# Kernel tuning notes

Hardware: AMD Instinct MI355X
Metric: run time of the kernel (lower is better)

Reference implementation:

```python
import jax, jax.numpy as jnp
import numpy as np

BATCH, SEQ, CH, ORDER = 4, 8192, 512, 64


def setup_inputs() -> dict:
    key = jax.random.key(0)
    k1, k2, k3 = jax.random.split(key, 3)
    x = jax.random.normal(k1, (BATCH, SEQ, CH), dtype=jnp.float32)
    # RTF parameters: small init so the denominator polynomial 1 + sum a_i z^-i
    # stays well-conditioned (stable transfer function), as in the FSSM init.
    A = 0.01 * jax.random.normal(k2, (CH, ORDER), dtype=jnp.float32)
    B = 0.01 * jax.random.normal(k3, (CH, ORDER), dtype=jnp.float32)
    h0 = jnp.zeros((1,), dtype=jnp.float32)
    return {"x": x, "A": A, "B": B, "h0": h0}


def _rtf_kernel(A, B, L):
    # Evaluate H(z) = b(z)/a(z) at the L roots of unity, then irfft -> impulse response.
    C = A.shape[0]
    a = jnp.concatenate([jnp.ones((C, 1), A.dtype), A], axis=-1)  # (C, N+1), leading coeff 1
    a_f = jnp.fft.rfft(a, n=L, axis=-1)                           # (C, L//2+1)
    b_f = jnp.fft.rfft(B, n=L, axis=-1)
    return jnp.fft.irfft(b_f / a_f, n=L, axis=-1)                 # (C, L)


def reference(x, A, B, h0):
    Bt, L, C = x.shape
    K = _rtf_kernel(A, B, L)                                      # (C, L)
    n_fft = 2 * L                                                 # causal (linear) convolution
    x_f = jnp.fft.rfft(x, n=n_fft, axis=1)                        # (B, n_fft//2+1, C)
    k_f = jnp.fft.rfft(K, n=n_fft, axis=-1).T[None]               # (1, n_fft//2+1, C)
    h1 = jnp.fft.irfft(x_f * k_f, n=n_fft, axis=1)[:, :L]         # (B, L, C)
    y1 = h1 + h0 * x
    return jax.nn.gelu(y1)
```

## Files before the change

kernel.cpp:

```cpp
#include <hip/hip_runtime.h>
#include <stdint.h>

#define NBATCH 4
#define LSEQ   8192
#define CH     512
#define ORDER  64
#define KTAP   256

typedef _Float16 half8 __attribute__((ext_vector_type(8)));
typedef _Float16 f16x2 __attribute__((ext_vector_type(2)));
typedef float    f32x4 __attribute__((ext_vector_type(4)));

#define NW    9
#define AFRAG_HALFS  ((size_t)CH * NW * 64 * 8)
#define WS_NEED      (AFRAG_HALFS * 2)

#define XSW   1320
#define XROWB 2640
#define LOW   260
#define LOWB  1040
#define SMEMB (16 * XROWB)

__device__ __forceinline__ uint32_t packh2(_Float16 lo, _Float16 hi) {
    f16x2 v; v.x = lo; v.y = hi;
    return __builtin_bit_cast(uint32_t, v);
}

__global__ __launch_bounds__(256) void rtf_afrag(const float* __restrict__ A,
                                                 const float* __restrict__ B,
                                                 const float* __restrict__ h0,
                                                 _Float16* __restrict__ afr) {
    __shared__ float Ksh[4][KTAP];
    const int wv = threadIdx.x >> 6, lane = threadIdx.x & 63;
    const int c  = blockIdx.x * 4 + wv;
    const float a  = A[c * ORDER + lane];
    const float bc = B[c * ORDER + lane];
    const float h0v = h0[0];
    float s = 0.0f;
    for (int t = 0; t < KTAP; ++t) {
        const float s1 = __shfl(s, 0);
        const float bt = (t < ORDER) ? __shfl(bc, t) : 0.0f;
        const float y  = bt + s1;
        float su = __shfl_down(s, 1);
        if (lane == ORDER - 1) su = 0.0f;
        s = su - a * y;
        if (lane == 0) Ksh[wv][t] = (t == 0) ? (y + h0v) : y;
    }
    __syncthreads();
    const int i = lane & 15, g = lane >> 4;
    for (int w = 0; w < NW; ++w) {
        half8 hv;
#pragma unroll
        for (int e = 0; e < 8; ++e) {
            const int t = 32 * w + 15 + i - 8 * g - e;
            hv[e] = (_Float16)((t >= 0 && t < KTAP) ? Ksh[wv][t] : 0.0f);
        }
        *reinterpret_cast<half8*>(afr + ((size_t)(c * NW + w) * 64 + lane) * 8) = hv;
    }
}

__global__ __launch_bounds__(256) void fir_mfma(const float* __restrict__ x,
                                                const _Float16* __restrict__ afr,
                                                float* __restrict__ out) {
    __shared__ __align__(16) char smem[SMEMB];
    const int gid     = blockIdx.x;
    const int logical = (gid & 7) * 128 + (gid >> 3);
    const int chgrp   = logical >> 5;
    const int rem     = logical & 31;
    const int bb      = rem >> 3;
    const int tg      = rem & 7;
    const int n0      = tg * 1024;

    {
        const int cg = threadIdx.x & 3;
        const int pr = threadIdx.x >> 2;
        const float* xsrc = x + (size_t)bb * LSEQ * CH + chgrp * 16 + cg * 4;
#pragma unroll
        for (int it = 0; it < 11; ++it) {
            const int p = pr + 64 * it;
            if (p < 656) {
                const int r0 = n0 - 271 + 2 * p;
                float4 v0 = {0.f, 0.f, 0.f, 0.f}, v1 = v0;
                if (r0 >= 0 && r0 < LSEQ)
                    v0 = *reinterpret_cast<const float4*>(xsrc + (size_t)r0 * CH);
                if (r0 + 1 >= 0 && r0 + 1 < LSEQ)
                    v1 = *reinterpret_cast<const float4*>(xsrc + (size_t)(r0 + 1) * CH);
                char* base = smem + (size_t)(cg * 4) * XROWB + 4 * p;
                *reinterpret_cast<uint32_t*>(base + 0 * XROWB) =
                    packh2((_Float16)v0.x, (_Float16)v1.x);
                *reinterpret_cast<uint32_t*>(base + 1 * XROWB) =
                    packh2((_Float16)v0.y, (_Float16)v1.y);
                *reinterpret_cast<uint32_t*>(base + 2 * XROWB) =
                    packh2((_Float16)v0.z, (_Float16)v1.z);
                *reinterpret_cast<uint32_t*>(base + 3 * XROWB) =
                    packh2((_Float16)v0.w, (_Float16)v1.w);
            }
        }
    }
    __syncthreads();

    const int wid = threadIdx.x >> 6, lane = threadIdx.x & 63;
    const int j = lane & 15, g = lane >> 4;
    const int c0 = chgrp * 16 + wid * 4;
    const _Float16* af = afr + (size_t)lane * 8;

    f32x4 acc[4][4];
#pragma unroll
    for (int ti = 0; ti < 4; ++ti)
#pragma unroll
        for (int q = 0; q < 4; ++q) acc[ti][q] = (f32x4){0.f, 0.f, 0.f, 0.f};

#pragma unroll
    for (int w = 0; w < NW; ++w) {
        half8 a[4];
#pragma unroll
        for (int q = 0; q < 4; ++q)
            a[q] = *reinterpret_cast<const half8*>(af + (size_t)((c0 + q) * NW + w) * 512);
        const int base = 16 * j + 8 * g - 32 * w + 256;
#pragma unroll
        for (int ti = 0; ti < 4; ++ti) {
#pragma unroll
            for (int q = 0; q < 4; ++q) {
                const half8 bv = *reinterpret_cast<const half8*>(
                    smem + (size_t)(wid * 4 + q) * XROWB + 2 * (base + 256 * ti));
                acc[ti][q] = __builtin_amdgcn_mfma_f32_16x16x32_f16(a[q], bv, acc[ti][q], 0, 0, 0);
            }
        }
    }

    const int cq = threadIdx.x & 3;
    const int nq = threadIdx.x >> 2;
#pragma unroll
    for (int ti = 0; ti < 4; ++ti) {
        __syncthreads();
#pragma unroll
        for (int q = 0; q < 4; ++q) {
            f32x4 o;
#pragma unroll
            for (int r = 0; r < 4; ++r) {
                const float y  = acc[ti][q][r];
                const float m2 = y * y;
                const float wv = fmaf(m2, 0.14270963f, 1.5957691f);
                const float e  = __expf(y * wv);
                const float rc = __builtin_amdgcn_rcpf(e + 1.0f);
                o[r] = y - y * rc;
            }
            *reinterpret_cast<f32x4*>(smem + (size_t)(wid * 4 + q) * LOWB
                                      + 4 * (16 * j + 4 * g)) = o;
        }
        __syncthreads();
        float* ob = out + ((size_t)bb * LSEQ + n0 + ti * 256) * CH + chgrp * 16 + cq * 4;
#pragma unroll
        for (int it = 0; it < 4; ++it) {
            const int n = nq + 64 * it;
            float4 o;
            o.x = *reinterpret_cast<float*>(smem + (size_t)(cq * 4 + 0) * LOWB + 4 * n);
            o.y = *reinterpret_cast<float*>(smem + (size_t)(cq * 4 + 1) * LOWB + 4 * n);
            o.z = *reinterpret_cast<float*>(smem + (size_t)(cq * 4 + 2) * LOWB + 4 * n);
            o.w = *reinterpret_cast<float*>(smem + (size_t)(cq * 4 + 3) * LOWB + 4 * n);
            *reinterpret_cast<float4*>(ob + (size_t)n * CH) = o;
        }
    }
}

#define RINGF 32
#define CPBF  256
__global__ __launch_bounds__(ORDER) void rtf_impulse_fb(const float* __restrict__ A,
                                                        const float* __restrict__ B,
                                                        const float* __restrict__ h0,
                                                        float* __restrict__ kt4) {
    const int c = blockIdx.x, lane = threadIdx.x;
    const float a = A[c * ORDER + lane], bc = B[c * ORDER + lane], h0v = h0[0];
    float s = 0.0f;
    for (int t = 0; t < KTAP; ++t) {
        const float s1 = __shfl(s, 0);
        const float bt = (t < ORDER) ? __shfl(bc, t) : 0.0f;
        const float y  = bt + s1;
        float su = __shfl_down(s, 1);
        if (lane == ORDER - 1) su = 0.0f;
        s = su - a * y;
        if (lane == 0) kt4[((size_t)(t >> 2) * CH + c) * 4 + (t & 3)] = (t == 0) ? (y + h0v) : y;
    }
}
__global__ __launch_bounds__(CPBF) void fir_gelu_fb(const float* __restrict__ x,
                                                    const float* __restrict__ kt4,
                                                    float* __restrict__ out) {
    const int h = blockIdx.x;
    const int logical = ((h & 7) << 8) | (h >> 3);
    const int tile = logical & 255, sl = logical >> 8;
    const int cb = sl & 1, b = sl >> 1;
    const int c = cb * CPBF + threadIdx.x;
    const int n0 = tile * RINGF;
    const float* xb = x + (size_t)b * LSEQ * CH + c;
    const float4* kt4v = (const float4*)kt4;
    float acc[RINGF]; float ring[RINGF]; float px[2][8]; float kbuf[2][8];
#pragma unroll
    for (int r = 0; r < RINGF; ++r) acc[r] = 0.0f;
#pragma unroll
    for (int i = 0; i < RINGF; ++i) ring[i] = xb[(size_t)(n0 + i) * CH];
    {
        const float4 ka = kt4v[(size_t)0 * CH + c];
        const float4 kb = kt4v[(size_t)1 * CH + c];
        kbuf[0][0] = ka.x; kbuf[0][1] = ka.y; kbuf[0][2] = ka.z; kbuf[0][3] = ka.w;
        kbuf[0][4] = kb.x; kbuf[0][5] = kb.y; kbuf[0][6] = kb.z; kbuf[0][7] = kb.w;
#pragma unroll
        for (int g2 = 0; g2 < 8; ++g2) {
            const int m = n0 - 1 - g2;
            px[0][g2] = (m >= 0) ? xb[(size_t)m * CH] : 0.0f;
        }
    }
    for (int tb = 0; tb < KTAP; tb += RINGF) {
#pragma unroll
        for (int q = 0; q < 4; ++q) {
            const int cur = q & 1, nxt = cur ^ 1;
            const int tn = tb + 8 * (q + 1);
            if (tn < KTAP) {
                const float4 ka = kt4v[(size_t)(tn >> 2) * CH + c];
                const float4 kb = kt4v[(size_t)((tn >> 2) + 1) * CH + c];
                kbuf[nxt][0] = ka.x; kbuf[nxt][1] = ka.y; kbuf[nxt][2] = ka.z; kbuf[nxt][3] = ka.w;
                kbuf[nxt][4] = kb.x; kbuf[nxt][5] = kb.y; kbuf[nxt][6] = kb.z; kbuf[nxt][7] = kb.w;
#pragma unroll
                for (int g2 = 0; g2 < 8; ++g2) {
                    const int m = n0 - tn - 1 - g2;
                    px[nxt][g2] = (m >= 0) ? xb[(size_t)m * CH] : 0.0f;
                }
            }
#pragma unroll
            for (int g2 = 0; g2 < 8; ++g2) {
                const int tq = 8 * q + g2;
                const float kv = kbuf[cur][g2];
#pragma unroll
                for (int r = 0; r < RINGF; ++r)
                    acc[r] = fmaf(kv, ring[(r - tq) & (RINGF - 1)], acc[r]);
                ring[(RINGF - 1 - tq) & (RINGF - 1)] = px[cur][g2];
            }
        }
    }
    float* ob = out + ((size_t)b * LSEQ + n0) * CH + c;
#pragma unroll
    for (int r = 0; r < RINGF; ++r) {
        const float y = acc[r];
        const float m2 = y * y;
        const float wv = fmaf(m2, 0.14270963f, 1.5957691f);
        const float e = __expf(y * wv);
        const float rc = __builtin_amdgcn_rcpf(e + 1.0f);
        ob[(size_t)r * CH] = y - y * rc;
    }
}

extern "C" void kernel_launch(void* const* d_in, const int* in_sizes, int n_in,
                              void* d_out, int out_size, void* d_ws, size_t ws_size,
                              hipStream_t stream) {
    const float* x  = (const float*)d_in[0];
    const float* A  = (const float*)d_in[1];
    const float* B  = (const float*)d_in[2];
    const float* h0 = (const float*)d_in[3];
    float* out = (float*)d_out;

    if (ws_size >= WS_NEED) {
        _Float16* afr = (_Float16*)d_ws;
        rtf_afrag<<<dim3(CH / 4), dim3(256), 0, stream>>>(A, B, h0, afr);
        fir_mfma<<<dim3(1024), dim3(256), 0, stream>>>(x, afr, out);
    } else {
        float* kt4 = (float*)d_ws;
        rtf_impulse_fb<<<dim3(CH), dim3(ORDER), 0, stream>>>(A, B, h0, kt4);
        fir_gelu_fb<<<dim3((LSEQ / RINGF) * (CH / CPBF) * NBATCH), dim3(CPBF), 0, stream>>>(x, kt4, out);
    }
}
```

Baseline: 63.79 us.

## Replace FIR MFMA kernel with persistent 256-block kernel streaming x tiles

The 1024-block FIR kernel becomes a 256-block, 512-thread kernel. Each block covers a 4096-sample half of the sequence for 16 channels, so the 271-sample halo is loaded once per half instead of once per 1024-sample tile. Filter fragments are held in registers across 16 output tiles. The front of the x window is staged up front, and the rest is prefetched into registers and written to LDS one chunk per output-tile iteration, overlapping global loads with MFMA and GELU work. Conversion uses the packed round-toward-zero fp16 instruction. The risks are fewer blocks (one wave of 256 CTAs with large LDS, about 156 KB each), less parallelism on a 256-CU device, and possible staging-order hazards if later tiles read LDS rows that have not been written yet.

```diff
diff --git a/kernel.cpp b/kernel.cpp
--- a/kernel.cpp
+++ b/kernel.cpp
@@ -6,23 +6,26 @@
 #define CH     512
 #define ORDER  64
 #define KTAP   256
+#define NW     9
 
 typedef _Float16 half8 __attribute__((ext_vector_type(8)));
-typedef _Float16 f16x2 __attribute__((ext_vector_type(2)));
+typedef __fp16   fp16x2 __attribute__((ext_vector_type(2)));
 typedef float    f32x4 __attribute__((ext_vector_type(4)));
 
-#define NW    9
 #define AFRAG_HALFS  ((size_t)CH * NW * 64 * 8)
 #define WS_NEED      (AFRAG_HALFS * 2)
 
-#define XSW   1320
-#define XROWB 2640
-#define LOW   260
+#define ROWS  4368
+#define XW    4376
+#define XWB   8752
+#define LOUT_OFF (16 * XWB)
 #define LOWB  1040
-#define SMEMB (16 * XROWB)
-
-__device__ __forceinline__ uint32_t packh2(_Float16 lo, _Float16 hi) {
-    f16x2 v; v.x = lo; v.y = hi;
+#define SMEMB (LOUT_OFF + 16 * LOWB)
+#define S1_PAIRS 1216
+#define PAIRS_TOT 2184
+
+__device__ __forceinline__ uint32_t pkrtz(float lo, float hi) {
+    fp16x2 v = __builtin_amdgcn_cvt_pkrtz(lo, hi);
     return __builtin_bit_cast(uint32_t, v);
 }
 
@@ -59,107 +62,132 @@
     }
 }
 
-__global__ __launch_bounds__(256) void fir_mfma(const float* __restrict__ x,
-                                                const _Float16* __restrict__ afr,
-                                                float* __restrict__ out) {
+__global__ __launch_bounds__(512) void fir_persist(const float* __restrict__ x,
+                                                   const _Float16* __restrict__ afr,
+                                                   float* __restrict__ out) {
     __shared__ __align__(16) char smem[SMEMB];
-    const int gid     = blockIdx.x;
-    const int logical = (gid & 7) * 128 + (gid >> 3);
-    const int chgrp   = logical >> 5;
-    const int rem     = logical & 31;
-    const int bb      = rem >> 3;
-    const int tg      = rem & 7;
-    const int n0      = tg * 1024;
-
+    const int bid   = blockIdx.x;
+    const int chgrp = bid & 31;
+    const int slice = bid >> 5;
+    const int nh    = slice & 1;
+    const int bb    = slice >> 1;
+    const int nbase = nh * 4096;
+    const int c0    = chgrp * 16;
+
+    const int wid  = threadIdx.x >> 6;
+    const int lane = threadIdx.x & 63;
+    const int ca   = c0 + 2 * wid;
+    const int cb_  = ca + 1;
+
+    half8 afA[NW], afB[NW];
+#pragma unroll
+    for (int w = 0; w < NW; ++w) {
+        afA[w] = *reinterpret_cast<const half8*>(afr + (((size_t)ca  * NW + w) * 64 + lane) * 8);
+        afB[w] = *reinterpret_cast<const half8*>(afr + (((size_t)cb_ * NW + w) * 64 + lane) * 8);
+    }
+
+    const int q  = threadIdx.x & 3;
+    const int pr = threadIdx.x >> 2;
+    const float* xsrc = x + (size_t)bb * LSEQ * CH + c0 + q * 4;
+    f32x4 L0[10], L1[10];
+#pragma unroll
+    for (int i = 0; i < 10; ++i) {
+        const int p  = pr + 128 * i;
+        const int r0 = nbase - 271 + 2 * p;
+        f32x4 z = {0.f, 0.f, 0.f, 0.f};
+        L0[i] = z; L1[i] = z;
+        if (p < S1_PAIRS) {
+            if ((unsigned)r0 < LSEQ)       L0[i] = *reinterpret_cast<const f32x4*>(xsrc + (size_t)r0 * CH);
+            if ((unsigned)(r0 + 1) < LSEQ) L1[i] = *reinterpret_cast<const f32x4*>(xsrc + (size_t)(r0 + 1) * CH);
+        }
+    }
+    f32x4 s0 = {0.f, 0.f, 0.f, 0.f}, s1 = s0;
     {
-        const int cg = threadIdx.x & 3;
-        const int pr = threadIdx.x >> 2;
-        const float* xsrc = x + (size_t)bb * LSEQ * CH + chgrp * 16 + cg * 4;
-#pragma unroll
-        for (int it = 0; it < 11; ++it) {
-            const int p = pr + 64 * it;
-            if (p < 656) {
-                const int r0 = n0 - 271 + 2 * p;
-                float4 v0 = {0.f, 0.f, 0.f, 0.f}, v1 = v0;
-                if (r0 >= 0 && r0 < LSEQ)
-                    v0 = *reinterpret_cast<const float4*>(xsrc + (size_t)r0 * CH);
-                if (r0 + 1 >= 0 && r0 + 1 < LSEQ)
-                    v1 = *reinterpret_cast<const float4*>(xsrc + (size_t)(r0 + 1) * CH);
-                char* base = smem + (size_t)(cg * 4) * XROWB + 4 * p;
-                *reinterpret_cast<uint32_t*>(base + 0 * XROWB) =
-                    packh2((_Float16)v0.x, (_Float16)v1.x);
-                *reinterpret_cast<uint32_t*>(base + 1 * XROWB) =
-                    packh2((_Float16)v0.y, (_Float16)v1.y);
-                *reinterpret_cast<uint32_t*>(base + 2 * XROWB) =
-                    packh2((_Float16)v0.z, (_Float16)v1.z);
-                *reinterpret_cast<uint32_t*>(base + 3 * XROWB) =
-                    packh2((_Float16)v0.w, (_Float16)v1.w);
-            }
+        const int p  = S1_PAIRS + pr;
+        const int r0 = nbase - 271 + 2 * p;
+        if ((unsigned)r0 < LSEQ)       s0 = *reinterpret_cast<const f32x4*>(xsrc + (size_t)r0 * CH);
+        if ((unsigned)(r0 + 1) < LSEQ) s1 = *reinterpret_cast<const f32x4*>(xsrc + (size_t)(r0 + 1) * CH);
+    }
+#pragma unroll
+    for (int i = 0; i < 10; ++i) {
+        const int p = pr + 128 * i;
+        if (p < S1_PAIRS) {
+            char* wb = smem + (size_t)(4 * q) * XWB + 4 * p;
+            *reinterpret_cast<uint32_t*>(wb + 0 * XWB) = pkrtz(L0[i][0], L1[i][0]);
+            *reinterpret_cast<uint32_t*>(wb + 1 * XWB) = pkrtz(L0[i][1], L1[i][1]);
+            *reinterpret_cast<uint32_t*>(wb + 2 * XWB) = pkrtz(L0[i][2], L1[i][2]);
+            *reinterpret_cast<uint32_t*>(wb + 3 * XWB) = pkrtz(L0[i][3], L1[i][3]);
         }
     }
     __syncthreads();
 
-    const int wid = threadIdx.x >> 6, lane = threadIdx.x & 63;
-    const int j = lane & 15, g = lane >> 4;
-    const int c0 = chgrp * 16 + wid * 4;
-    const _Float16* af = afr + (size_t)lane * 8;
-
-    f32x4 acc[4][4];
-#pragma unroll
-    for (int ti = 0; ti < 4; ++ti)
-#pragma unroll
-        for (int q = 0; q < 4; ++q) acc[ti][q] = (f32x4){0.f, 0.f, 0.f, 0.f};
-
-#pragma unroll
-    for (int w = 0; w < NW; ++w) {
-        half8 a[4];
-#pragma unroll
-        for (int q = 0; q < 4; ++q)
-            a[q] = *reinterpret_cast<const half8*>(af + (size_t)((c0 + q) * NW + w) * 512);
-        const int base = 16 * j + 8 * g - 32 * w + 256;
-#pragma unroll
-        for (int ti = 0; ti < 4; ++ti) {
-#pragma unroll
-            for (int q = 0; q < 4; ++q) {
-                const half8 bv = *reinterpret_cast<const half8*>(
-                    smem + (size_t)(wid * 4 + q) * XROWB + 2 * (base + 256 * ti));
-                acc[ti][q] = __builtin_amdgcn_mfma_f32_16x16x32_f16(a[q], bv, acc[ti][q], 0, 0, 0);
-            }
-        }
-    }
-
-    const int cq = threadIdx.x & 3;
-    const int nq = threadIdx.x >> 2;
-#pragma unroll
-    for (int ti = 0; ti < 4; ++ti) {
+    const int jb = 16 * (lane & 15);
+    const int gb = 8 * (lane >> 4);
+    const char* xrowA = smem + (size_t)(2 * wid + 0) * XWB;
+    const char* xrowB = smem + (size_t)(2 * wid + 1) * XWB;
+    float* loutA = reinterpret_cast<float*>(smem + LOUT_OFF + (size_t)(2 * wid + 0) * LOWB);
+    float* loutB = reinterpret_cast<float*>(smem + LOUT_OFF + (size_t)(2 * wid + 1) * LOWB);
+    const int nf  = jb + 4 * (lane >> 4);
+    const int cq  = threadIdx.x & 3;
+    const int nr0 = threadIdx.x >> 2;
+
+    for (int ti = 0; ti < 16; ++ti) {
+        if (ti < 8) {
+            const int p = S1_PAIRS + 128 * ti + pr;
+            if (p < PAIRS_TOT) {
+                char* wb = smem + (size_t)(4 * q) * XWB + 4 * p;
+                *reinterpret_cast<uint32_t*>(wb + 0 * XWB) = pkrtz(s0[0], s1[0]);
+                *reinterpret_cast<uint32_t*>(wb + 1 * XWB) = pkrtz(s0[1], s1[1]);
+                *reinterpret_cast<uint32_t*>(wb + 2 * XWB) = pkrtz(s0[2], s1[2]);
+                *reinterpret_cast<uint32_t*>(wb + 3 * XWB) = pkrtz(s0[3], s1[3]);
+            }
+            if (ti < 7) {
+                const int pn = S1_PAIRS + 128 * (ti + 1) + pr;
+                const int r0 = nbase - 271 + 2 * pn;
+                f32x4 z = {0.f, 0.f, 0.f, 0.f}; s0 = z; s1 = z;
+                if (pn < PAIRS_TOT) {
+                    if ((unsigned)r0 < LSEQ)       s0 = *reinterpret_cast<const f32x4*>(xsrc + (size_t)r0 * CH);
+                    if ((unsigned)(r0 + 1) < LSEQ) s1 = *reinterpret_cast<const f32x4*>(xsrc + (size_t)(r0 + 1) * CH);
+                }
+            }
+        }
+        f32x4 aca = {0.f, 0.f, 0.f, 0.f}, acb = aca;
+        const int bbase = 512 * ti + 2 * (jb + gb + 256);
+#pragma unroll
+        for (int w = 0; w < NW; ++w) {
+            const int byt = bbase - 64 * w;
+            const half8 bva = *reinterpret_cast<const half8*>(xrowA + byt);
+            const half8 bvb = *reinterpret_cast<const half8*>(xrowB + byt);
+            aca = __builtin_amdgcn_mfma_f32_16x16x32_f16(afA[w], bva, aca, 0, 0, 0);
+            acb = __builtin_amdgcn_mfma_f32_16x16x32_f16(afB[w], bvb, acb, 0, 0, 0);
+        }
+        f32x4 oa, ob;
+#pragma unroll
+        for (int r = 0; r < 4; ++r) {
+            float y  = aca[r];
+            float wv = fmaf(y * y, 0.14270963f, 1.5957691f);
+            float e  = __expf(y * wv);
+            oa[r] = y - y * __builtin_amdgcn_rcpf(e + 1.0f);
+            y  = acb[r];
+            wv = fmaf(y * y, 0.14270963f, 1.5957691f);
+            e  = __expf(y * wv);
+            ob[r] = y - y * __builtin_amdgcn_rcpf(e + 1.0f);
+        }
+        *reinterpret_cast<f32x4*>(loutA + nf) = oa;
+        *reinterpret_cast<f32x4*>(loutB + nf) = ob;
         __syncthreads();
-#pragma unroll
-        for (int q = 0; q < 4; ++q) {
+        float* obp = out + ((size_t)bb * LSEQ + nbase + 256 * ti) * CH + c0 + 4 * cq;
+#pragma unroll
+        for (int pass = 0; pass < 2; ++pass) {
+            const int nr = nr0 + 128 * pass;
             f32x4 o;
-#pragma unroll
-            for (int r = 0; r < 4; ++r) {
-                const float y  = acc[ti][q][r];
-                const float m2 = y * y;
-                const float wv = fmaf(m2, 0.14270963f, 1.5957691f);
-                const float e  = __expf(y * wv);
-                const float rc = __builtin_amdgcn_rcpf(e + 1.0f);
-                o[r] = y - y * rc;
-            }
-            *reinterpret_cast<f32x4*>(smem + (size_t)(wid * 4 + q) * LOWB
-                                      + 4 * (16 * j + 4 * g)) = o;
+            o[0] = *reinterpret_cast<const float*>(smem + LOUT_OFF + (size_t)(4 * cq + 0) * LOWB + 4 * nr);
+            o[1] = *reinterpret_cast<const float*>(smem + LOUT_OFF + (size_t)(4 * cq + 1) * LOWB + 4 * nr);
+            o[2] = *reinterpret_cast<const float*>(smem + LOUT_OFF + (size_t)(4 * cq + 2) * LOWB + 4 * nr);
+            o[3] = *reinterpret_cast<const float*>(smem + LOUT_OFF + (size_t)(4 * cq + 3) * LOWB + 4 * nr);
+            *reinterpret_cast<f32x4*>(obp + (size_t)nr * CH) = o;
         }
         __syncthreads();
-        float* ob = out + ((size_t)bb * LSEQ + n0 + ti * 256) * CH + chgrp * 16 + cq * 4;
-#pragma unroll
-        for (int it = 0; it < 4; ++it) {
-            const int n = nq + 64 * it;
-            float4 o;
-            o.x = *reinterpret_cast<float*>(smem + (size_t)(cq * 4 + 0) * LOWB + 4 * n);
-            o.y = *reinterpret_cast<float*>(smem + (size_t)(cq * 4 + 1) * LOWB + 4 * n);
-            o.z = *reinterpret_cast<float*>(smem + (size_t)(cq * 4 + 2) * LOWB + 4 * n);
-            o.w = *reinterpret_cast<float*>(smem + (size_t)(cq * 4 + 3) * LOWB + 4 * n);
-            *reinterpret_cast<float4*>(ob + (size_t)n * CH) = o;
-        }
     }
 }
 
@@ -211,9 +239,9 @@
     }
     for (int tb = 0; tb < KTAP; tb += RINGF) {
 #pragma unroll
-        for (int q = 0; q < 4; ++q) {
-            const int cur = q & 1, nxt = cur ^ 1;
-            const int tn = tb + 8 * (q + 1);
+        for (int qq = 0; qq < 4; ++qq) {
+            const int cur = qq & 1, nxt = cur ^ 1;
+            const int tn = tb + 8 * (qq + 1);
             if (tn < KTAP) {
                 const float4 ka = kt4v[(size_t)(tn >> 2) * CH + c];
                 const float4 kb = kt4v[(size_t)((tn >> 2) + 1) * CH + c];
@@ -227,7 +255,7 @@
             }
 #pragma unroll
             for (int g2 = 0; g2 < 8; ++g2) {
-                const int tq = 8 * q + g2;
+                const int tq = 8 * qq + g2;
                 const float kv = kbuf[cur][g2];
 #pragma unroll
                 for (int r = 0; r < RINGF; ++r)
@@ -240,11 +268,9 @@
 #pragma unroll
     for (int r = 0; r < RINGF; ++r) {
         const float y = acc[r];
-        const float m2 = y * y;
-        const float wv = fmaf(m2, 0.14270963f, 1.5957691f);
+        const float wv = fmaf(y * y, 0.14270963f, 1.5957691f);
         const float e = __expf(y * wv);
-        const float rc = __builtin_amdgcn_rcpf(e + 1.0f);
-        ob[(size_t)r * CH] = y - y * rc;
+        ob[(size_t)r * CH] = y - y * __builtin_amdgcn_rcpf(e + 1.0f);
     }
 }
 
@@ -260,7 +286,7 @@
     if (ws_size >= WS_NEED) {
         _Float16* afr = (_Float16*)d_ws;
         rtf_afrag<<<dim3(CH / 4), dim3(256), 0, stream>>>(A, B, h0, afr);
-        fir_mfma<<<dim3(1024), dim3(256), 0, stream>>>(x, afr, out);
+        fir_persist<<<dim3(256), dim3(512), 0, stream>>>(x, afr, out);
     } else {
         float* kt4 = (float*)d_ws;
         rtf_impulse_fb<<<dim3(CH), dim3(ORDER), 0, stream>>>(A, B, h0, kt4);
```

Result: faster. 61.61 us (-3.4%).
